# Kernel tuning notes

Hardware: AMD Instinct MI355X
Metric: run time of the kernel (lower is better)

The kernel has to match this reference:

```python
import jax, jax.numpy as jnp
import numpy as np

B, N, DIM, H, DH = 2, 1024, 2048, 16, 128
MAX_POS = 16
QK_SCALE = 10.0  # qk_norm_scale (replaces dim_head**-0.5 when qk_norm=True)
NEG = -1e30  # large negative mask value (sigmoid -> 0, softmax -> 0)

def rotate_half(x):
    # interleaved pair rotation: '... (d r) -> ... d r', r=2
    shape = x.shape
    xr = x.reshape(shape[:-1] + (shape[-1] // 2, 2))
    x1, x2 = xr[..., 0], xr[..., 1]
    return jnp.stack((-x2, x1), axis=-1).reshape(shape)

def setup_inputs() -> dict:
    key = jax.random.key(0)
    ks = jax.random.split(key, 10)
    # proper rotary frequencies, repeat-interleaved to match rotate_half's pair layout
    half = DH // 2
    inv_freq = 1.0 / (10000.0 ** (np.arange(half, dtype=np.float32) / half))
    freqs = np.repeat(np.outer(np.arange(N, dtype=np.float32), inv_freq), 2, axis=-1)  # [N, DH]
    sd = 0.02
    return {
        'x': jax.random.normal(ks[0], (B, N, DIM), jnp.float32),
        'rotary_freqs': jnp.asarray(freqs),
        'w_q': jax.random.normal(ks[1], (DIM, H * DH), jnp.float32) * sd,
        'w_k': jax.random.normal(ks[2], (DIM, H * DH), jnp.float32) * sd,
        'w_v': jax.random.normal(ks[3], (DIM, H * DH), jnp.float32) * sd,
        'cope_emb': jax.random.normal(ks[4], (MAX_POS, DH), jnp.float32) * sd,  # CoPE pos_emb (nonzero for testing)
        'th_pre': jnp.eye(H, dtype=jnp.float32) + jax.random.normal(ks[5], (H, H), jnp.float32) * sd,
        'th_post': jnp.eye(H, dtype=jnp.float32) + jax.random.normal(ks[6], (H, H), jnp.float32) * sd,
        'w_vgate': jax.random.normal(ks[7], (DIM, H * DH), jnp.float32) * sd,
        'b_vgate': jnp.full((H * DH,), 10.0, jnp.float32),
        'w_hgate': jax.random.normal(ks[8], (DIM, H), jnp.float32) * sd,
        'b_hgate': jnp.full((H,), 10.0, jnp.float32),
        'w_out': jax.random.normal(ks[9], (H * DH, DIM), jnp.float32) * sd,
    }

def reference(x, rotary_freqs, w_q, w_k, w_v, cope_emb, th_pre, th_post, w_vgate, b_vgate, w_hgate, b_hgate, w_out):
    b, n, _ = x.shape
    to_heads = lambda t: t.reshape(b, n, H, DH).transpose(0, 2, 1, 3)  # b h n d
    q = to_heads(x @ w_q)
    k = to_heads(x @ w_k)
    v = to_heads(x @ w_v)
    # qk l2-norm (groups=1), then fixed qk_norm_scale
    q = q / jnp.maximum(jnp.linalg.norm(q, axis=-1, keepdims=True), 1e-12)
    k = k / jnp.maximum(jnp.linalg.norm(k, axis=-1, keepdims=True), 1e-12)
    # rotary embedding (scale=1, rot_dim == dim_head)
    cos, sin = jnp.cos(rotary_freqs), jnp.sin(rotary_freqs)
    q = q * cos + rotate_half(q) * sin
    k = k * cos + rotate_half(k) * sin
    sim = jnp.einsum('bhid,bhjd->bhij', q, k) * QK_SCALE
    sim = jnp.einsum('hg,bgij->bhij', th_pre, sim)  # pre-softmax talking heads (1x1 conv over heads)
    causal = jnp.triu(jnp.ones((n, n), dtype=bool), 1)
    sim = jnp.where(causal, NEG, sim)
    # ---- CoPE (linear interpolation path) ----
    gates = jax.nn.sigmoid(sim)  # masked entries -> 0
    pos = jnp.flip(jnp.cumsum(jnp.flip(gates, -1), axis=-1), -1)  # reverse cumsum over j
    pos = jnp.minimum(pos, MAX_POS - 1.0)
    logits_int = jnp.einsum('bhnd,pd->bhnp', q, cope_emb)
    pos_floor = jnp.floor(pos)
    w_interp = pos - pos_floor
    lc = jnp.take_along_axis(logits_int, jnp.ceil(pos).astype(jnp.int32), axis=-1)
    lf = jnp.take_along_axis(logits_int, pos_floor.astype(jnp.int32), axis=-1)
    sim = sim + lc * w_interp + lf * (1.0 - w_interp)
    # ------------------------------------------
    attn = jax.nn.softmax(sim, axis=-1)
    attn = jnp.einsum('hg,bgij->bhij', th_post, attn)  # post-softmax talking heads
    out = jnp.einsum('bhij,bhjd->bhid', attn, v)
    # per-head value gate
    head_gate = jax.nn.sigmoid(x @ w_hgate + b_hgate)  # b n h
    out = out * head_gate.transpose(0, 2, 1)[..., None]
    out = out.transpose(0, 2, 1, 3).reshape(b, n, H * DH)
    # elementwise value gate (sigmoid, bias init 10)
    out = out * jax.nn.sigmoid(x @ w_vgate + b_vgate)
    return out @ w_out
```

## Files before the change

### kernel.cpp

```cpp
#include <hip/hip_runtime.h>
#include <hip/hip_fp16.h>

typedef unsigned short u16;
typedef __attribute__((ext_vector_type(4))) float f32x4;
typedef __attribute__((ext_vector_type(8))) _Float16 f16x8;
typedef __attribute__((ext_vector_type(4))) _Float16 f16x4;
typedef __attribute__((ext_vector_type(8))) unsigned short u16x8;
typedef __attribute__((ext_vector_type(4))) unsigned short u16x4;

#define DEVI __device__ __forceinline__
#define MASKV (-1000.0f)

DEVI u16 f2h(float f){ __half h = __float2half(f); return __half_as_ushort(h); }
DEVI float h2f(u16 v){ return __half2float(__ushort_as_half(v)); }
DEVI float sigm(float s){ float e = __expf(-fabsf(s)); return (s >= 0.f) ? 1.f/(1.f+e) : e/(1.f+e); }

DEVI void async16(const void* g, void* l){
  __builtin_amdgcn_global_load_lds((__attribute__((address_space(1))) const unsigned int*)g,
                                   (__attribute__((address_space(3))) unsigned int*)l, 16, 0, 0);
}

struct PrepArgs {
  const float* src[7];
  u16* dst[7];
  int C[7];
};
__global__ __launch_bounds__(256) void k_prep(PrepArgs p){
  __shared__ u16 t[64][65];
  int z = blockIdx.z;
  int tid = threadIdx.x;
  if (z == 0){
    size_t b0 = (size_t)(blockIdx.y*32 + blockIdx.x)*4096;
    #pragma unroll
    for (int c = 0; c < 4; c++){
      size_t ix = b0 + (size_t)(c*256 + tid)*4;
      f32x4 v = *(const f32x4*)(p.src[0] + ix);
      u16x4 o;
      #pragma unroll
      for (int e=0; e<4; e++) o[e] = f2h(v[e]);
      *(u16x4*)(p.dst[0] + ix) = o;
    }
    return;
  }
  const float* src = p.src[z]; u16* dst = p.dst[z];
  int C = p.C[z];
  int c0 = blockIdx.x*64, r0 = blockIdx.y*64;
  if (c0 >= C) return;
  int tx = tid & 15, ty = tid >> 4;
  #pragma unroll
  for (int rr = 0; rr < 4; rr++){
    int r = r0 + rr*16 + ty, c = c0 + tx*4;
    if (c < C){
      f32x4 v = *(const f32x4*)(src + (size_t)r*C + c);
      #pragma unroll
      for (int e=0; e<4; e++) t[rr*16+ty][tx*4+e] = f2h(v[e]);
    }
  }
  __syncthreads();
  #pragma unroll
  for (int rr = 0; rr < 4; rr++){
    int rr2 = c0 + rr*16 + ty;
    if (rr2 < C){
      u16x4 o;
      #pragma unroll
      for (int e=0; e<4; e++) o[e] = t[tx*4+e][rr*16+ty];
      *(u16x4*)(dst + (size_t)rr2*2048 + r0 + tx*4) = o;
    }
  }
}

__global__ __launch_bounds__(256) void k_transpose_h(const u16* __restrict__ src, u16* __restrict__ dst,
    int R, int C, long sps, long dps){
  __shared__ u16 t[32][33];
  src += (size_t)blockIdx.z * sps; dst += (size_t)blockIdx.z * dps;
  int c0 = blockIdx.x*32, r0 = blockIdx.y*32;
  int tx = threadIdx.x & 31, ty = threadIdx.x >> 5;
  #pragma unroll
  for (int i = ty; i < 32; i += 8){
    int r = r0 + i, c = c0 + tx;
    if (r < R && c < C) t[i][tx] = src[(size_t)r*C + c];
  }
  __syncthreads();
  #pragma unroll
  for (int i = ty; i < 32; i += 8){
    int rr = c0 + i, cc = r0 + tx;
    if (rr < C && cc < R) dst[(size_t)rr*R + cc] = t[tx][i];
  }
}

struct ProjArgs {
  const u16* xh;
  const u16* wT0; const u16* wT1; const u16* wT2; const u16* wT3;
  u16* q; u16* k; u16* v; u16* vg;
  const float* bvg;
};
__global__ __launch_bounds__(512) void k_proj2(ProjArgs p){
  __shared__ __align__(16) u16 ldsA[3][8192];
  __shared__ __align__(16) u16 ldsB[3][8192];
  const int z = blockIdx.z;
  const u16* wT = (z==0) ? p.wT0 : (z==1) ? p.wT1 : (z==2) ? p.wT2 : p.wT3;
  const int m0 = blockIdx.y << 8, n0 = blockIdx.x << 8;
  const int tid = threadIdx.x, w = tid >> 6, l = tid & 63;
  const int wm = w >> 2, wn = w & 3, qq = l >> 4, m = l & 15;
  const u16* aS = p.xh + (size_t)(m0 + w*32 + (l>>2)) * 2048 + (l&3)*8;
  const u16* bS = wT   + (size_t)(n0 + w*32 + (l>>2)) * 2048 + (l&3)*8;

  f32x4 acc[8][4];
  { f32x4 zr = {0.f,0.f,0.f,0.f};
    #pragma unroll
    for (int i=0;i<8;i++)
      #pragma unroll
      for (int j=0;j<4;j++) acc[i][j] = zr; }

#define STG(buf,kt) do{ \
    async16(aS + (size_t)(kt)*32,           &ldsA[buf][(w*32)*32]); \
    async16(aS + (size_t)16*2048 + (size_t)(kt)*32, &ldsA[buf][(w*32+16)*32]); \
    async16(bS + (size_t)(kt)*32,           &ldsB[buf][(w*32)*32]); \
    async16(bS + (size_t)16*2048 + (size_t)(kt)*32, &ldsB[buf][(w*32+16)*32]); }while(0)

#define SEGBODY(cur) do{ \
    f16x8 bf0 = *(const f16x8*)(&ldsB[cur][(wn*64 +  0 + m)*32 + qq*8]); \
    f16x8 bf1 = *(const f16x8*)(&ldsB[cur][(wn*64 + 16 + m)*32 + qq*8]); \
    f16x8 bf2 = *(const f16x8*)(&ldsB[cur][(wn*64 + 32 + m)*32 + qq*8]); \
    f16x8 bf3 = *(const f16x8*)(&ldsB[cur][(wn*64 + 48 + m)*32 + qq*8]); \
    _Pragma("unroll") \
    for (int i=0;i<8;i++){ \
      f16x8 a = *(const f16x8*)(&ldsA[cur][(wm*128 + i*16 + m)*32 + qq*8]); \
      acc[i][0] = __builtin_amdgcn_mfma_f32_16x16x32_f16(a, bf0, acc[i][0], 0,0,0); \
      acc[i][1] = __builtin_amdgcn_mfma_f32_16x16x32_f16(a, bf1, acc[i][1], 0,0,0); \
      acc[i][2] = __builtin_amdgcn_mfma_f32_16x16x32_f16(a, bf2, acc[i][2], 0,0,0); \
      acc[i][3] = __builtin_amdgcn_mfma_f32_16x16x32_f16(a, bf3, acc[i][3], 0,0,0); \
    } }while(0)

  STG(0,0); STG(1,1);
  asm volatile("s_waitcnt vmcnt(4)" ::: "memory");
  __builtin_amdgcn_s_barrier();

  int cur = 0;
  for (int t = 0; t < 62; t++){
    int nb = (cur == 0) ? 2 : cur - 1;
    STG(nb, t+2);
    SEGBODY(cur);
    asm volatile("s_waitcnt vmcnt(4)" ::: "memory");
    __builtin_amdgcn_s_barrier();
    cur = (cur == 2) ? 0 : cur + 1;
  }
  SEGBODY(cur);
  asm volatile("s_waitcnt vmcnt(0)" ::: "memory");
  __builtin_amdgcn_s_barrier();
  cur = (cur == 2) ? 0 : cur + 1;
  SEGBODY(cur);

  u16* dst3 = (z==0) ? p.q : (z==1) ? p.k : p.v;
  #pragma unroll
  for (int i=0;i<8;i++)
  #pragma unroll
  for (int j=0;j<4;j++)
  #pragma unroll
  for (int r=0;r<4;r++){
    int gr = m0 + wm*128 + i*16 + qq*4 + r;
    int gc = n0 + wn*64 + j*16 + m;
    float v = acc[i][j][r];
    if (z == 3){
      p.vg[(size_t)gr*2048 + gc] = f2h(sigm(v + p.bvg[gc]));
    } else {
      int b = gr >> 10, ii = gr & 1023, h = gc >> 7, d = gc & 127;
      dst3[(((size_t)(b*16 + h))*1024 + ii)*128 + d] = f2h(v);
    }
  }
#undef STG
#undef SEGBODY
}

__global__ __launch_bounds__(256) void k_hgate(const u16* __restrict__ xh, const u16* __restrict__ whgT,
    const float* __restrict__ bhg, float* __restrict__ hg){
  __shared__ float red[4][256];
  int tid = threadIdx.x, w = tid>>6, l = tid&63, q = l>>4, m = l&15;
  int t0 = blockIdx.x*16;
  f32x4 acc = {0.f,0.f,0.f,0.f};
  const u16* xr = xh   + (size_t)(t0 + m)*2048 + w*512;
  const u16* br = whgT + (size_t)m*2048 + w*512;
  #pragma unroll 4
  for (int k = 0; k < 512; k += 32){
    f16x8 a = *(const f16x8*)(xr + k + q*8);
    f16x8 b = *(const f16x8*)(br + k + q*8);
    acc = __builtin_amdgcn_mfma_f32_16x16x32_f16(a, b, acc, 0, 0, 0);
  }
  #pragma unroll
  for (int r = 0; r < 4; r++) red[w][(q*4+r)*16 + m] = acc[r];
  __syncthreads();
  float v = red[0][tid] + red[1][tid] + red[2][tid] + red[3][tid];
  int tl = tid >> 4, h = tid & 15;
  hg[(size_t)(t0 + tl)*16 + h] = sigm(v + bhg[h]);
}

__global__ __launch_bounds__(256) void k_normrope(u16* __restrict__ qb, u16* __restrict__ kb,
    const float* __restrict__ freqs, const float* __restrict__ cope, float* __restrict__ L){
  __shared__ float ce[2048];
  int tid = threadIdx.x;
  for (int i2 = tid; i2 < 2048; i2 += 256) ce[i2] = cope[i2];
  __syncthreads();
  int w = tid >> 6, l = tid & 63;
  int r = blockIdx.x*4 + w;
  int isq = (r < 32768) ? 1 : 0;
  int rr = isq ? r : r - 32768;
  int i = rr & 1023;
  u16* base = (isq ? qb : kb) + (size_t)rr*128;
  float v0 = h2f(base[2*l]), v1 = h2f(base[2*l+1]);
  float ss = v0*v0 + v1*v1;
  #pragma unroll
  for (int off = 1; off < 64; off <<= 1) ss += __shfl_xor(ss, off);
  float rn = 1.f / fmaxf(sqrtf(ss), 1e-12f);
  v0 *= rn; v1 *= rn;
  float f = freqs[i*128 + 2*l];
  float sn, cs; sincosf(f, &sn, &cs);
  float o0 = v0*cs - v1*sn, o1 = v1*cs + v0*sn;
  base[2*l] = f2h(o0); base[2*l+1] = f2h(o1);
  if (isq){
    #pragma unroll
    for (int p = 0; p < 16; p++){
      float part = o0*ce[p*128 + 2*l] + o1*ce[p*128 + 2*l + 1];
      #pragma unroll
      for (int off = 1; off < 64; off <<= 1) part += __shfl_xor(part, off);
      if (l == p) L[(size_t)rr*16 + p] = part;
    }
  }
}

__global__ __launch_bounds__(256) void k_qk(const u16* __restrict__ qb, const u16* __restrict__ kb,
    u16* __restrict__ S){
  __shared__ __align__(16) u16 As[8192];
  __shared__ __align__(16) u16 Bs[16384];
  int bh = blockIdx.y;
  int bx = 15 - (int)blockIdx.x;
  int i0 = bx*64, it = bx >> 1;
  int njt = (bx + 2) >> 1;
  int tid = threadIdx.x, w = tid>>6, l = tid&63, q = l>>4, m = l&15, wm = w&1, wn = w>>1;
  const u16* qbase = qb + (size_t)bh*131072;
  const u16* kbase = kb + (size_t)bh*131072;
  #pragma unroll
  for (int sub = 0; sub < 4; sub++){
    int row = w*16 + (l>>2);
    async16(qbase + (size_t)(i0 + row)*128 + sub*32 + (l&3)*8, As + sub*2048 + (w*16)*32);
  }
  u16* dstbase = S + ((size_t)bh*36 + (it*(it+1))/2)*16384 + (size_t)((bx&1)*64)*128;
  for (int jt = 0; jt < njt; jt++){
    __syncthreads();
    #pragma unroll
    for (int sub = 0; sub < 4; sub++)
      #pragma unroll
      for (int p = 0; p < 2; p++){
        int row = w*32 + p*16 + (l>>2);
        async16(kbase + (size_t)(jt*128 + row)*128 + sub*32 + (l&3)*8,
                Bs + sub*4096 + (w*32 + p*16)*32);
      }
    __syncthreads();
    f32x4 acc[2][4];
    { f32x4 z = {0.f,0.f,0.f,0.f};
      #pragma unroll
      for (int a2=0;a2<2;a2++)
        #pragma unroll
        for (int b2=0;b2<4;b2++) acc[a2][b2] = z; }
    #pragma unroll
    for (int kc = 0; kc < 4; kc++){
      f16x8 af[2], bf[4];
      #pragma unroll
      for (int t = 0; t < 2; t++) af[t] = *(const f16x8*)(As + kc*2048 + (wm*32 + t*16 + m)*32 + q*8);
      #pragma unroll
      for (int t = 0; t < 4; t++) bf[t] = *(const f16x8*)(Bs + kc*4096 + (wn*64 + t*16 + m)*32 + q*8);
      #pragma unroll
      for (int a2 = 0; a2 < 2; a2++)
        #pragma unroll
        for (int b2 = 0; b2 < 4; b2++)
          acc[a2][b2] = __builtin_amdgcn_mfma_f32_16x16x32_f16(af[a2], bf[b2], acc[a2][b2], 0, 0, 0);
    }
    u16* dst = dstbase + (size_t)jt*16384;
    #pragma unroll
    for (int ti=0; ti<2; ti++)
    #pragma unroll
    for (int tj=0; tj<4; tj++)
    #pragma unroll
    for (int r=0; r<4; r++){
      int iloc = wm*32 + ti*16 + q*4 + r;
      int jloc = wn*64 + tj*16 + m;
      float v = acc[ti][tj][r] * 10.f;
      if (jt*128 + jloc > i0 + iloc) v = MASKV;
      dst[(size_t)iloc*128 + jloc] = f2h(v);
    }
  }
}

struct CopeArgs { const u16* S; const float* L; const float* thpre; u16* Sout; float* ml; };
__global__ __launch_bounds__(1024) void k_cope(CopeArgs pa){
  __shared__ u16 raw[16*276];
  __shared__ float thsh[256];
  __shared__ float Lsh[1024];
  int b = blockIdx.y;
  int i0 = (int)(gridDim.x - 1 - blockIdx.x) * 4;
  int tid = threadIdx.x, w = tid>>6, l = tid&63;
  int h = w;
  if (tid < 256) thsh[tid] = pa.thpre[tid];
  Lsh[tid] = pa.L[ ((size_t)((b*16 + (tid>>6))*1024) + i0 + ((tid>>4)&3))*16 + (tid&15) ];
  __syncthreads();
  float th_r[16];
  #pragma unroll
  for (int g = 0; g < 16; g++) th_r[g] = thsh[h*16 + g];
  int ii = l >> 4, j0 = (l & 15)*4;
  int i = i0 + ii, it1 = i >> 7, iloc = i & 127;
  const float* Lrow = Lsh + h*64 + ii*16;
  float carry = 0.f, mrun = -1e30f, lrun = 0.f;
  int tmax = (i0 + 3) >> 6;
  for (int t = tmax; t >= 0; t--){
    int jt1 = (t*64) >> 7, jo = (t*64) & 127;
    __syncthreads();
    {
      int e = tid*4;
      int g = e >> 8, r = e & 255;
      int si = r >> 6, j = r & 63;
      int irow = i0 + si; int it2 = irow >> 7, il2 = irow & 127;
      const u16* src = pa.S + ((size_t)((b*16+g)*36 + (it2*(it2+1))/2 + jt1))*16384
                           + (size_t)il2*128 + jo + j;
      *(u16x4*)(raw + g*276 + si*68 + j) = *(const u16x4*)src;
    }
    __syncthreads();
    float s0=0.f, s1=0.f, s2=0.f, s3=0.f;
    #pragma unroll
    for (int g = 0; g < 16; g++){
      u16x4 v = *(const u16x4*)(raw + g*276 + ii*68 + j0);
      float tg = th_r[g];
      s0 += tg*h2f(v[0]); s1 += tg*h2f(v[1]); s2 += tg*h2f(v[2]); s3 += tg*h2f(v[3]);
    }
    float g0 = sigm(s0), g1 = sigm(s1), g2 = sigm(s2), g3 = sigm(s3);
    float c3 = g3, c2 = g2 + c3, c1 = g1 + c2, c0 = g0 + c1;
    float T = c0, Tacc = T;
    #pragma unroll
    for (int off = 1; off < 16; off <<= 1){
      float tv = __shfl(Tacc, (l + off) & 63);
      if (((l & 15) + off) < 16) Tacc += tv;
    }
    float Rh = Tacc - T;
    float rowtot = __shfl(Tacc, l & 48);
    float sf[4];
    float cc[4] = {c0, c1, c2, c3};
    float ssv[4] = {s0, s1, s2, s3};
    #pragma unroll
    for (int c = 0; c < 4; c++){
      float pos = fminf(cc[c] + Rh + carry, 15.f);
      float pf = floorf(pos);
      float wi = pos - pf;
      int ic = (int)ceilf(pos), ifl = (int)pf;
      float v = ssv[c] + Lrow[ic]*wi + Lrow[ifl]*(1.f - wi);
      sf[c] = v;
    }
    carry += rowtot;
    u16x4 ov;
    #pragma unroll
    for (int c = 0; c < 4; c++){ ov[c] = f2h(sf[c]); sf[c] = h2f(ov[c]); }
    *(u16x4*)(pa.Sout + ((size_t)((b*16+h)*36 + (it1*(it1+1))/2 + jt1))*16384
              + (size_t)iloc*128 + jo + j0) = ov;
    float M = fmaxf(fmaxf(sf[0], sf[1]), fmaxf(sf[2], sf[3]));
    #pragma unroll
    for (int off = 1; off < 16; off <<= 1) M = fmaxf(M, __shfl_xor(M, off));
    float mnew = fmaxf(mrun, M);
    float es = __expf(fminf(sf[0]-mnew,0.f)) + __expf(fminf(sf[1]-mnew,0.f))
             + __expf(fminf(sf[2]-mnew,0.f)) + __expf(fminf(sf[3]-mnew,0.f));
    #pragma unroll
    for (int off = 1; off < 16; off <<= 1) es += __shfl_xor(es, off);
    lrun = lrun*__expf(fminf(mrun - mnew, 0.f)) + es;
    mrun = mnew;
  }
  if ((l & 15) == 0){
    size_t bix = (size_t)(b*16 + h)*1024 + i0 + ii;
    pa.ml[bix] = mrun;
    pa.ml[32768 + bix] = 1.f/fmaxf(lrun, 1e-30f);
  }
}

struct PostArgs { const u16* S; const float* ml; const float* thpost; u16* Sout; };
__global__ __launch_bounds__(256) void k_postmix(PostArgs pa){
  __shared__ u16 at[16*1040];
  __shared__ _Float16 thsh[256];
  __shared__ float mh[128], rlh[128];
  int tile = blockIdx.x >> 4, sub = blockIdx.x & 15, b = blockIdx.y;
  int it = 0;
  #pragma unroll
  for (int t2=1; t2<8; t2++) if (tile >= (t2*(t2+1))/2) it = t2;
  int tid = threadIdx.x;
  thsh[tid] = (_Float16)pa.thpost[tid];
  if (tid < 128){
    int g = tid >> 3, ii = tid & 7;
    size_t ix = (size_t)(b*16+g)*1024 + it*128 + sub*8 + ii;
    mh[tid] = pa.ml[ix]; rlh[tid] = pa.ml[32768 + ix];
  }
  __syncthreads();
  {
    int g = tid >> 4, l16 = tid & 15;
    const u16* src = pa.S + ((size_t)((b*16+g)*36 + tile))*16384 + sub*1024;
    #pragma unroll
    for (int c = 0; c < 16; c++){
      int e = c*64 + l16*4;
      int ii = e >> 7;
      float mm = mh[g*8+ii], rr = rlh[g*8+ii];
      u16x4 sv = *(const u16x4*)(src + e);
      u16x4 o;
      #pragma unroll
      for (int z2=0; z2<4; z2++) o[z2] = f2h(__expf(fminf(h2f(sv[z2]) - mm, 0.f)) * rr);
      *(u16x4*)(at + g*1040 + e) = o;
    }
  }
  __syncthreads();
  int h = tid >> 4, c16 = tid & 15;
  _Float16 th_h[16];
  #pragma unroll
  for (int g = 0; g < 16; g++) th_h[g] = thsh[h*16 + g];
  u16* dst = pa.Sout + ((size_t)((b*16+h)*36 + tile))*16384 + sub*1024;
  #pragma unroll
  for (int k = 0; k < 16; k++){
    int e = c16*4 + k*64;
    f16x4 a = {0,0,0,0};
    #pragma unroll
    for (int g = 0; g < 16; g++){
      f16x4 v = *(const f16x4*)(at + g*1040 + e);
      a += v * th_h[g];
    }
    *(f16x4*)(dst + e) = a;
  }
}

struct PvArgs { const u16* S; const u16* vT; const float* hg; const u16* vg; u16* gated; };
__global__ __launch_bounds__(256) void k_pv(PvArgs pa){
  __shared__ __align__(16) u16 As[8192];
  __shared__ __align__(16) u16 Bs[16384];
  int bh = blockIdx.y, b = bh >> 4, h = bh & 15;
  int bx = 15 - (int)blockIdx.x;
  int i0 = bx*64, it = bx >> 1;
  int nc = (bx + 2) >> 1;
  int tid = threadIdx.x, w = tid>>6, l = tid&63, q = l>>4, m = l&15, wm = w&1, wn = w>>1;
  const u16* abase = pa.S + ((size_t)bh*36 + (it*(it+1))/2)*16384 + (size_t)((bx&1)*64)*128;
  const u16* vt    = pa.vT + (size_t)bh*131072;
  f32x4 acc[2][4];
  { f32x4 z = {0.f,0.f,0.f,0.f};
    #pragma unroll
    for (int a2=0;a2<2;a2++)
      #pragma unroll
      for (int b2=0;b2<4;b2++) acc[a2][b2] = z; }
  for (int jc = 0; jc < nc; jc++){
    __syncthreads();
    #pragma unroll
    for (int sub = 0; sub < 4; sub++){
      int row = w*16 + (l>>2);
      async16(abase + (size_t)jc*16384 + (size_t)row*128 + sub*32 + (l&3)*8,
              As + sub*2048 + (w*16)*32);
      #pragma unroll
      for (int p = 0; p < 2; p++){
        int brow = w*32 + p*16 + (l>>2);
        async16(vt + (size_t)brow*1024 + jc*128 + sub*32 + (l&3)*8,
                Bs + sub*4096 + (w*32 + p*16)*32);
      }
    }
    __syncthreads();
    #pragma unroll
    for (int kc = 0; kc < 4; kc++){
      f16x8 af[2], bf[4];
      #pragma unroll
      for (int t = 0; t < 2; t++) af[t] = *(const f16x8*)(As + kc*2048 + (wm*32 + t*16 + m)*32 + q*8);
      #pragma unroll
      for (int t = 0; t < 4; t++) bf[t] = *(const f16x8*)(Bs + kc*4096 + (wn*64 + t*16 + m)*32 + q*8);
      #pragma unroll
      for (int a2 = 0; a2 < 2; a2++)
        #pragma unroll
        for (int b2 = 0; b2 < 4; b2++)
          acc[a2][b2] = __builtin_amdgcn_mfma_f32_16x16x32_f16(af[a2], bf[b2], acc[a2][b2], 0, 0, 0);
    }
  }
  #pragma unroll
  for (int ti=0; ti<2; ti++)
  #pragma unroll
  for (int tj=0; tj<4; tj++)
  #pragma unroll
  for (int r=0; r<4; r++){
    int i = i0 + wm*32 + ti*16 + q*4 + r;
    int d = wn*64 + tj*16 + m;
    int tok = b*1024 + i;
    float v = acc[ti][tj][r] * pa.hg[(size_t)tok*16 + h] * h2f(pa.vg[(size_t)tok*2048 + h*128 + d]);
    if (v != v) v = 333.f;
    pa.gated[(size_t)tok*2048 + h*128 + d] = f2h(v);
  }
}

__global__ __launch_bounds__(256) void k_out(const u16* __restrict__ gated, const u16* __restrict__ woT,
    float* __restrict__ out){
  __shared__ __align__(16) u16 As[2048];
  __shared__ __align__(16) u16 Bs[4096];
  int bx = blockIdx.x;
  int by = blockIdx.y;
  int trow0 = by*64, c0 = bx*128;
  int tid = threadIdx.x, w = tid>>6, l = tid&63, q = l>>4, m = l&15, wm = w&1, wn = w>>1;
  f32x4 acc[2][4];
  { f32x4 z = {0.f,0.f,0.f,0.f};
    #pragma unroll
    for (int a2=0;a2<2;a2++)
      #pragma unroll
      for (int b2=0;b2<4;b2++) acc[a2][b2] = z; }
  for (int k0 = 0; k0 < 2048; k0 += 32){
    __syncthreads();
    {
      int row = w*16 + (l>>2);
      async16(gated + (size_t)(trow0 + row)*2048 + k0 + (l&3)*8, As + (w*16)*32);
    }
    #pragma unroll
    for (int p = 0; p < 2; p++){
      int row = w*32 + p*16 + (l>>2);
      async16(woT + (size_t)(c0 + row)*2048 + k0 + (l&3)*8, Bs + (w*32 + p*16)*32);
    }
    __syncthreads();
    f16x8 af[2], bf[4];
    #pragma unroll
    for (int t = 0; t < 2; t++) af[t] = *(const f16x8*)(As + (wm*32 + t*16 + m)*32 + q*8);
    #pragma unroll
    for (int t = 0; t < 4; t++) bf[t] = *(const f16x8*)(Bs + (wn*64 + t*16 + m)*32 + q*8);
    #pragma unroll
    for (int a2 = 0; a2 < 2; a2++)
      #pragma unroll
      for (int b2 = 0; b2 < 4; b2++)
        acc[a2][b2] = __builtin_amdgcn_mfma_f32_16x16x32_f16(af[a2], bf[b2], acc[a2][b2], 0, 0, 0);
  }
  #pragma unroll
  for (int ti=0; ti<2; ti++)
  #pragma unroll
  for (int tj=0; tj<4; tj++)
  #pragma unroll
  for (int r=0; r<4; r++){
    int trow = trow0 + wm*32 + ti*16 + q*4 + r;
    int col  = c0 + wn*64 + tj*16 + m;
    float o = acc[ti][tj][r];
    if (o != o) o = 911.f;
    out[(size_t)trow*2048 + col] = o;
  }
}

extern "C" void kernel_launch(void* const* d_in, const int* in_sizes, int n_in,
                              void* d_out, int out_size, void* d_ws, size_t ws_size,
                              hipStream_t stream){
  const float* x      = (const float*)d_in[0];
  const float* freqs  = (const float*)d_in[1];
  const float* w_q    = (const float*)d_in[2];
  const float* w_k    = (const float*)d_in[3];
  const float* w_v    = (const float*)d_in[4];
  const float* cope   = (const float*)d_in[5];
  const float* thpre  = (const float*)d_in[6];
  const float* thpost = (const float*)d_in[7];
  const float* w_vg   = (const float*)d_in[8];
  const float* b_vg   = (const float*)d_in[9];
  const float* w_hg   = (const float*)d_in[10];
  const float* b_hg   = (const float*)d_in[11];
  const float* w_out  = (const float*)d_in[12];

  char* ws = (char*)d_ws;
  size_t off = 0;
  auto alloc = [&](size_t bytes)->char*{ char* r = ws + off; off += (bytes + 255) & ~(size_t)255; return r; };
  u16*   xh    = (u16*)  alloc(8388608);
  u16*   wqT   = (u16*)  alloc(8388608);
  u16*   wkT   = (u16*)  alloc(8388608);
  u16*   wvT   = (u16*)  alloc(8388608);
  u16*   wvgT  = (u16*)  alloc(8388608);
  u16*   woT   = (u16*)  alloc(8388608);
  u16*   whgT  = (u16*)  alloc(65536);
  u16*   qb    = (u16*)  alloc(8388608);
  u16*   kb    = (u16*)  alloc(8388608);
  u16*   vb    = (u16*)  alloc(8388608);
  u16*   vTT   = (u16*)  alloc(8388608);
  u16*   vg    = (u16*)  alloc(8388608);
  u16*   gated = (u16*)  alloc(8388608);
  float* L     = (float*)alloc(2097152);
  float* hg    = (float*)alloc(131072);
  float* ml    = (float*)alloc(262144);
  u16*   S     = (u16*)  alloc(37748736);

  dim3 b256(256);
  PrepArgs pp;
  pp.src[0]=x;    pp.dst[0]=xh;   pp.C[0]=2048;
  pp.src[1]=w_q;  pp.dst[1]=wqT;  pp.C[1]=2048;
  pp.src[2]=w_k;  pp.dst[2]=wkT;  pp.C[2]=2048;
  pp.src[3]=w_v;  pp.dst[3]=wvT;  pp.C[3]=2048;
  pp.src[4]=w_vg; pp.dst[4]=wvgT; pp.C[4]=2048;
  pp.src[5]=w_out;pp.dst[5]=woT;  pp.C[5]=2048;
  pp.src[6]=w_hg; pp.dst[6]=whgT; pp.C[6]=16;
  k_prep<<<dim3(32,32,7), b256, 0, stream>>>(pp);

  ProjArgs pa{ xh, wqT, wkT, wvT, wvgT, qb, kb, vb, vg, b_vg };
  k_proj2<<<dim3(8,8,4), dim3(512), 0, stream>>>(pa);
  k_hgate<<<dim3(128), b256, 0, stream>>>(xh, whgT, b_hg, hg);
  k_transpose_h<<<dim3(4,32,32), b256, 0, stream>>>(vb, vTT, 1024, 128, 131072L, 131072L);
  k_normrope<<<dim3(16384), b256, 0, stream>>>(qb, kb, freqs, cope, L);
  k_qk<<<dim3(16,32), b256, 0, stream>>>(qb, kb, S);
  CopeArgs ca{ S, L, thpre, S, ml };
  k_cope<<<dim3(256,2), dim3(1024), 0, stream>>>(ca);
  PostArgs po{ S, ml, thpost, S };
  k_postmix<<<dim3(576,2), b256, 0, stream>>>(po);
  PvArgs pv{ S, vTT, hg, vg, gated };
  k_pv<<<dim3(16,32), b256, 0, stream>>>(pv);
  k_out<<<dim3(16,32), b256, 0, stream>>>(gated, woT, (float*)d_out);
}
```

Before: 480.6 us.

## Retile projection GEMM to 128x256 blocks with swizzled LDS and MFMA priority

The QKV/value-gate projection GEMM moves from 256x256 tiles with 512 threads to 128x256 tiles with 256 threads. This doubles the block count to 512 so more blocks fill the CUs. The staging layout gains an XOR swizzle on the 16-byte column chunks to reduce LDS bank conflicts on the fragment reads. The MFMA section is wrapped in s_setprio to favour math waves. In exchange, A-tile reuse per block drops, so more B (weight) traffic reaches L2.

```diff
diff --git a/kernel.cpp b/kernel.cpp
--- a/kernel.cpp
+++ b/kernel.cpp
@@ -94,16 +94,23 @@
   u16* q; u16* k; u16* v; u16* vg;
   const float* bvg;
 };
-__global__ __launch_bounds__(512) void k_proj2(ProjArgs p){
-  __shared__ __align__(16) u16 ldsA[3][8192];
+__global__ __launch_bounds__(256) void k_proj2(ProjArgs p){
+  __shared__ __align__(16) u16 ldsA[3][4096];
   __shared__ __align__(16) u16 ldsB[3][8192];
   const int z = blockIdx.z;
   const u16* wT = (z==0) ? p.wT0 : (z==1) ? p.wT1 : (z==2) ? p.wT2 : p.wT3;
-  const int m0 = blockIdx.y << 8, n0 = blockIdx.x << 8;
-  const int tid = threadIdx.x, w = tid >> 6, l = tid & 63;
-  const int wm = w >> 2, wn = w & 3, qq = l >> 4, m = l & 15;
-  const u16* aS = p.xh + (size_t)(m0 + w*32 + (l>>2)) * 2048 + (l&3)*8;
-  const u16* bS = wT   + (size_t)(n0 + w*32 + (l>>2)) * 2048 + (l&3)*8;
+  const int m0 = blockIdx.y << 7, n0 = blockIdx.x << 8;
+  const int tid = threadIdx.x, wn = tid >> 6, l = tid & 63;
+  const int qq = l >> 4, m = l & 15;
+  const int sw = (qq ^ ((m >> 1) & 3)) * 8;
+  const int colsw = 8 * ((tid & 3) ^ ((tid >> 3) & 3));
+  const int r0 = tid >> 2;
+  const u16* aS0 = p.xh + (size_t)(m0 + r0) * 2048 + colsw;
+  const u16* aS1 = aS0 + (size_t)64 * 2048;
+  const u16* bS0 = wT   + (size_t)(n0 + r0) * 2048 + colsw;
+  const u16* bS1 = bS0 + (size_t)64 * 2048;
+  const u16* bS2 = bS0 + (size_t)128 * 2048;
+  const u16* bS3 = bS0 + (size_t)192 * 2048;
 
   f32x4 acc[8][4];
   { f32x4 zr = {0.f,0.f,0.f,0.f};
@@ -113,43 +120,47 @@
       for (int j=0;j<4;j++) acc[i][j] = zr; }
 
 #define STG(buf,kt) do{ \
-    async16(aS + (size_t)(kt)*32,           &ldsA[buf][(w*32)*32]); \
-    async16(aS + (size_t)16*2048 + (size_t)(kt)*32, &ldsA[buf][(w*32+16)*32]); \
-    async16(bS + (size_t)(kt)*32,           &ldsB[buf][(w*32)*32]); \
-    async16(bS + (size_t)16*2048 + (size_t)(kt)*32, &ldsB[buf][(w*32+16)*32]); }while(0)
-
-#define SEGBODY(cur) do{ \
-    f16x8 bf0 = *(const f16x8*)(&ldsB[cur][(wn*64 +  0 + m)*32 + qq*8]); \
-    f16x8 bf1 = *(const f16x8*)(&ldsB[cur][(wn*64 + 16 + m)*32 + qq*8]); \
-    f16x8 bf2 = *(const f16x8*)(&ldsB[cur][(wn*64 + 32 + m)*32 + qq*8]); \
-    f16x8 bf3 = *(const f16x8*)(&ldsB[cur][(wn*64 + 48 + m)*32 + qq*8]); \
+    async16(aS0 + (size_t)(kt)*32, &ldsA[buf][tid*8]); \
+    async16(aS1 + (size_t)(kt)*32, &ldsA[buf][tid*8 + 2048]); \
+    async16(bS0 + (size_t)(kt)*32, &ldsB[buf][tid*8]); \
+    async16(bS1 + (size_t)(kt)*32, &ldsB[buf][tid*8 + 2048]); \
+    async16(bS2 + (size_t)(kt)*32, &ldsB[buf][tid*8 + 4096]); \
+    async16(bS3 + (size_t)(kt)*32, &ldsB[buf][tid*8 + 6144]); }while(0)
+
+#define COMPUTE(buf) do{ \
+    f16x8 bf0 = *(const f16x8*)(&ldsB[buf][(wn*64 +  0 + m)*32 + sw]); \
+    f16x8 bf1 = *(const f16x8*)(&ldsB[buf][(wn*64 + 16 + m)*32 + sw]); \
+    f16x8 bf2 = *(const f16x8*)(&ldsB[buf][(wn*64 + 32 + m)*32 + sw]); \
+    f16x8 bf3 = *(const f16x8*)(&ldsB[buf][(wn*64 + 48 + m)*32 + sw]); \
+    __builtin_amdgcn_s_setprio(1); \
     _Pragma("unroll") \
-    for (int i=0;i<8;i++){ \
-      f16x8 a = *(const f16x8*)(&ldsA[cur][(wm*128 + i*16 + m)*32 + qq*8]); \
+    for (int i = 0; i < 8; i++){ \
+      f16x8 a = *(const f16x8*)(&ldsA[buf][(i*16 + m)*32 + sw]); \
       acc[i][0] = __builtin_amdgcn_mfma_f32_16x16x32_f16(a, bf0, acc[i][0], 0,0,0); \
       acc[i][1] = __builtin_amdgcn_mfma_f32_16x16x32_f16(a, bf1, acc[i][1], 0,0,0); \
       acc[i][2] = __builtin_amdgcn_mfma_f32_16x16x32_f16(a, bf2, acc[i][2], 0,0,0); \
       acc[i][3] = __builtin_amdgcn_mfma_f32_16x16x32_f16(a, bf3, acc[i][3], 0,0,0); \
-    } }while(0)
+    } \
+    __builtin_amdgcn_s_setprio(0); }while(0)
 
   STG(0,0); STG(1,1);
-  asm volatile("s_waitcnt vmcnt(4)" ::: "memory");
+  asm volatile("s_waitcnt vmcnt(6)" ::: "memory");
   __builtin_amdgcn_s_barrier();
 
   int cur = 0;
   for (int t = 0; t < 62; t++){
     int nb = (cur == 0) ? 2 : cur - 1;
     STG(nb, t+2);
-    SEGBODY(cur);
-    asm volatile("s_waitcnt vmcnt(4)" ::: "memory");
+    COMPUTE(cur);
+    asm volatile("s_waitcnt vmcnt(6)" ::: "memory");
     __builtin_amdgcn_s_barrier();
     cur = (cur == 2) ? 0 : cur + 1;
   }
-  SEGBODY(cur);
+  COMPUTE(cur);
   asm volatile("s_waitcnt vmcnt(0)" ::: "memory");
   __builtin_amdgcn_s_barrier();
   cur = (cur == 2) ? 0 : cur + 1;
-  SEGBODY(cur);
+  COMPUTE(cur);
 
   u16* dst3 = (z==0) ? p.q : (z==1) ? p.k : p.v;
   #pragma unroll
@@ -158,7 +169,7 @@
   for (int j=0;j<4;j++)
   #pragma unroll
   for (int r=0;r<4;r++){
-    int gr = m0 + wm*128 + i*16 + qq*4 + r;
+    int gr = m0 + i*16 + qq*4 + r;
     int gc = n0 + wn*64 + j*16 + m;
     float v = acc[i][j][r];
     if (z == 3){
@@ -169,7 +180,7 @@
     }
   }
 #undef STG
-#undef SEGBODY
+#undef COMPUTE
 }
 
 __global__ __launch_bounds__(256) void k_hgate(const u16* __restrict__ xh, const u16* __restrict__ whgT,
@@ -589,7 +600,7 @@
   k_prep<<<dim3(32,32,7), b256, 0, stream>>>(pp);
 
   ProjArgs pa{ xh, wqT, wkT, wvT, wvgT, qb, kb, vb, vg, b_vg };
-  k_proj2<<<dim3(8,8,4), dim3(512), 0, stream>>>(pa);
+  k_proj2<<<dim3(8,16,4), dim3(256), 0, stream>>>(pa);
   k_hgate<<<dim3(128), b256, 0, stream>>>(xh, whgT, b_hg, hg);
   k_transpose_h<<<dim3(4,32,32), b256, 0, stream>>>(vb, vTT, 1024, 128, 131072L, 131072L);
   k_normrope<<<dim3(16384), b256, 0, stream>>>(qb, kb, freqs, cope, L);
```

Result: no change. 483.5 us (+0.6%).
